# Kernel optimization log

Measured on AMD Instinct MI355X. Metric: run time of the kernel, lower is better.

## Reference

```python
import jax, jax.numpy as jnp
import numpy as np

N_NODES = 10000
N_EDGES = 640000
F_IN = 128
HID = 128
N_LAYERS = 3
N_ACT = 4096
NEG_SLOPE = 0.2


def setup_inputs() -> dict:
    key = jax.random.key(0)
    ks = jax.random.split(key, 16)
    s = 0.05
    return {
        "x": jax.random.normal(ks[0], (N_NODES, F_IN), jnp.float32),
        "edge_index": jax.random.randint(ks[1], (2, N_EDGES), 0, N_NODES, jnp.int64),
        "action_src": jax.random.randint(ks[2], (N_ACT,), 0, N_NODES, jnp.int64),
        "action_dst": jax.random.randint(ks[3], (N_ACT,), 0, N_NODES, jnp.int64),
        "action_type": jax.random.randint(ks[4], (N_ACT,), 0, 2, jnp.int32),
        "gat_W": jax.random.normal(ks[5], (N_LAYERS, HID, HID), jnp.float32) * s,
        "gat_asrc": jax.random.normal(ks[6], (N_LAYERS, HID), jnp.float32) * s,
        "gat_adst": jax.random.normal(ks[7], (N_LAYERS, HID), jnp.float32) * s,
        "gat_b": jax.random.normal(ks[8], (N_LAYERS, HID), jnp.float32) * s,
        "mlp_W1": jax.random.normal(ks[9], (2 * HID + 1, HID), jnp.float32) * s,
        "mlp_b1": jax.random.normal(ks[10], (HID,), jnp.float32) * s,
        "mlp_W2": jax.random.normal(ks[11], (HID, 1), jnp.float32) * s,
        "mlp_b2": jax.random.normal(ks[12], (1,), jnp.float32) * s,
    }


def _gat_layer(h, src, dst, W, a_src, a_dst, b, n_nodes):
    # PyG GATConv, heads=1: z = h W; e_ij = leaky_relu(a_src.z_j + a_dst.z_i)
    z = h @ W                                   # [N, HID]
    e = jax.nn.leaky_relu((z @ a_src)[src] + (z @ a_dst)[dst], NEG_SLOPE)  # [E+N]
    m = jax.ops.segment_max(e, dst, num_segments=n_nodes)
    m = jnp.where(jnp.isfinite(m), m, 0.0)
    ex = jnp.exp(e - m[dst])
    denom = jax.ops.segment_sum(ex, dst, num_segments=n_nodes)
    alpha = ex / denom[dst]                     # softmax over incoming edges
    out = jax.ops.segment_sum(alpha[:, None] * z[src], dst, num_segments=n_nodes)
    return out + b


def reference(x, edge_index, action_src, action_dst, action_type,
              gat_W, gat_asrc, gat_adst, gat_b,
              mlp_W1, mlp_b1, mlp_W2, mlp_b2):
    n = x.shape[0]
    loop = jnp.arange(n, dtype=edge_index.dtype)  # add_self_loops=True
    src = jnp.concatenate([edge_index[0], loop])
    dst = jnp.concatenate([edge_index[1], loop])
    h = x
    for l in range(N_LAYERS):
        h = jax.nn.relu(_gat_layer(h, src, dst, gat_W[l], gat_asrc[l], gat_adst[l], gat_b[l], n))
    # vectorized action scoring: [h[src], h[dst], type_flag] -> MLP -> scalar
    feat = jnp.concatenate(
        [h[action_src], h[action_dst], action_type.astype(h.dtype)[:, None]], axis=-1)
    hidden = jax.nn.relu(feat @ mlp_W1 + mlp_b1)
    scores = (hidden @ mlp_W2 + mlp_b2)[:, 0]   # [N_ACT]
    return scores
```

## Files before the change

kernel.cpp:

```cpp
#include <hip/hip_runtime.h>
#include <hip/hip_bf16.h>
#include <hip/hip_fp16.h>

#define N_NODES 10000
#define N_EDGES 640000
#define TOT_E   (N_EDGES + N_NODES)
#define HID     128
#define NEG_SLOPE 0.2f
#define N_ACT   4096

#define NBKT   250
#define NPB    40
#define P1_EPB 4096
#define P1_EPT 16
#define P1_BLOCKS 159
#define SLOTP  56
#define G_BLOCKS 313

__global__ __launch_bounds__(256) void part1_k(const int* __restrict__ ei,
                                               unsigned* __restrict__ bpart,
                                               int* __restrict__ bcnt) {
    __shared__ int hist[256];
    __shared__ int lofs[256];
    __shared__ int sc[256];
    __shared__ unsigned stage[P1_EPB];
    __shared__ unsigned char bkt_of[P1_EPB];
    int t = threadIdx.x;
    hist[t] = 0;
    __syncthreads();

    unsigned pk[P1_EPT];
    int bk[P1_EPT];
    int e0 = blockIdx.x * P1_EPB;
#pragma unroll
    for (int i = 0; i < P1_EPT; i++) {
        int e = e0 + i * 256 + t;
        if (e < TOT_E) {
            int src, dst;
            if (e < N_EDGES) { src = ei[e]; dst = ei[N_EDGES + e]; }
            else             { src = e - N_EDGES; dst = src; }
            pk[i] = ((unsigned)dst << 16) | (unsigned)src;
            bk[i] = dst / NPB;
            atomicAdd(&hist[bk[i]], 1);
        } else bk[i] = -1;
    }
    __syncthreads();
    int v = hist[t];
    sc[t] = v;
    __syncthreads();
    for (int o = 1; o < 256; o <<= 1) {
        int u = (t >= o) ? sc[t - o] : 0;
        __syncthreads();
        sc[t] += u;
        __syncthreads();
    }
    lofs[t] = sc[t] - v;
    bcnt[blockIdx.x * 256 + t] = v;
    hist[t] = 0;
    __syncthreads();
#pragma unroll
    for (int i = 0; i < P1_EPT; i++) {
        if (bk[i] >= 0) {
            int p = atomicAdd(&hist[bk[i]], 1);
            int slot = lofs[bk[i]] + p;
            stage[slot] = pk[i];
            bkt_of[slot] = (unsigned char)bk[i];
        }
    }
    __syncthreads();
    int nv = min(P1_EPB, TOT_E - e0);
    for (int s = t; s < nv; s += 256) {
        int b = bkt_of[s];
        bpart[b * (P1_BLOCKS * SLOTP) + blockIdx.x * SLOTP + (s - lofs[b])] = stage[s];
    }
}

__device__ __forceinline__ void agg_node(const __half2* __restrict__ z2,
                                         const float* __restrict__ zsi, float zdn,
                                         const int* __restrict__ csr, int o0, int deg,
                                         int lane, float& accx, float& accy, float& denom) {
    for (int base = 0; base < deg; base += 64) {
        int j = base + lane;
        int sreg = 0;
        float ex = 0.f;
        if (j < deg) {
            int s = csr[o0 + j];
            sreg = s;
            float e = zsi[s] + zdn;
            e = e > 0.f ? e : NEG_SLOPE * e;
            ex = __expf(e);
        }
        int cnt = min(64, deg - base);
        int nfull = cnt & ~7;
        int q = 0;
        if (nfull) {
            __half2 cur[8];
            float exc[8];
#pragma unroll
            for (int u = 0; u < 8; u++) {
                int sq = __builtin_amdgcn_readlane(sreg, u);
                exc[u] = __uint_as_float(
                    __builtin_amdgcn_readlane(__float_as_uint(ex), u));
                cur[u] = z2[sq * 64];
            }
            for (q = 8; q < nfull; q += 8) {
                __half2 nxt[8];
                float exn[8];
#pragma unroll
                for (int u = 0; u < 8; u++) {
                    int sq = __builtin_amdgcn_readlane(sreg, q + u);
                    exn[u] = __uint_as_float(
                        __builtin_amdgcn_readlane(__float_as_uint(ex), q + u));
                    nxt[u] = z2[sq * 64];
                }
#pragma unroll
                for (int u = 0; u < 8; u++) {
                    denom += exc[u];
                    float2 vf = __half22float2(cur[u]);
                    accx = fmaf(exc[u], vf.x, accx);
                    accy = fmaf(exc[u], vf.y, accy);
                    cur[u] = nxt[u];
                    exc[u] = exn[u];
                }
            }
#pragma unroll
            for (int u = 0; u < 8; u++) {
                denom += exc[u];
                float2 vf = __half22float2(cur[u]);
                accx = fmaf(exc[u], vf.x, accx);
                accy = fmaf(exc[u], vf.y, accy);
            }
            q = nfull;
        }
        for (; q < cnt; q++) {
            int sq = __builtin_amdgcn_readlane(sreg, q);
            float exq = __uint_as_float(
                __builtin_amdgcn_readlane(__float_as_uint(ex), q));
            denom += exq;
            float2 vf = __half22float2(z2[sq * 64]);
            accx = fmaf(exq, vf.x, accx);
            accy = fmaf(exq, vf.y, accy);
        }
    }
}

__device__ __forceinline__ void gload_lds16(const float* g, float* l) {
    __builtin_amdgcn_global_load_lds(
        (const __attribute__((address_space(1))) void*)g,
        (__attribute__((address_space(3))) void*)l, 16, 0, 0);
}

__global__ __launch_bounds__(256) void g2_k(const float* __restrict__ A,
                                            const float* __restrict__ W,
                                            const float* __restrict__ avs,
                                            const float* __restrict__ avd,
                                            __half* __restrict__ z16,
                                            float* __restrict__ zs,
                                            float* __restrict__ zd,
                                            const unsigned* __restrict__ bpart,
                                            const int* __restrict__ bcnt,
                                            int* __restrict__ csr,
                                            int* __restrict__ offs) {
    __shared__ float smem[20480];
    int t = threadIdx.x;

    if (blockIdx.x < G_BLOCKS) {
        float* As = smem;
        float* Ws = smem + 32 * HID;
        int w = t >> 6, lane = t & 63;
        int row0 = blockIdx.x * 32;
#pragma unroll
        for (int i = 0; i < 4; i++) {
            int chunk = w * 4 + i;
            long foff = (long)row0 * HID + chunk * 256;
            const float* g = ((foff + 256) <= (long)N_NODES * HID) ? (A + foff + lane * 4)
                                                                   : (A + lane * 4);
            gload_lds16(g, As + chunk * 256);
        }
#pragma unroll
        for (int i = 0; i < 16; i++) {
            int chunk = w * 16 + i;
            gload_lds16(W + chunk * 256 + lane * 4, Ws + chunk * 256);
        }
        __syncthreads();

        int tx = t & 31, ty = t >> 5;
        int r0 = ty * 4;
        float acc[4][4] = {{0.f}};
#pragma unroll 4
        for (int k4 = 0; k4 < 32; k4++) {
            float ak[4][4];
#pragma unroll
            for (int r = 0; r < 4; r++) {
                float4 a4 = *(const float4*)&As[(r0 + r) * HID + k4 * 4];
                ak[r][0] = a4.x; ak[r][1] = a4.y; ak[r][2] = a4.z; ak[r][3] = a4.w;
            }
            const float* Wb = &Ws[k4 * 4 * HID + tx * 4];
#pragma unroll
            for (int kk = 0; kk < 4; kk++) {
                float4 wv = *(const float4*)&Wb[kk * HID];
#pragma unroll
                for (int r = 0; r < 4; r++) {
                    acc[r][0] = fmaf(ak[r][kk], wv.x, acc[r][0]);
                    acc[r][1] = fmaf(ak[r][kk], wv.y, acc[r][1]);
                    acc[r][2] = fmaf(ak[r][kk], wv.z, acc[r][2]);
                    acc[r][3] = fmaf(ak[r][kk], wv.w, acc[r][3]);
                }
            }
        }
        float4 asv = *(const float4*)&avs[tx * 4];
        float4 adv = *(const float4*)&avd[tx * 4];
#pragma unroll
        for (int r = 0; r < 4; r++) {
            int row = row0 + r0 + r;
            if (row < N_NODES) {
                *(__half2*)&z16[row * HID + tx * 4]     = __floats2half2_rn(acc[r][0], acc[r][1]);
                *(__half2*)&z16[row * HID + tx * 4 + 2] = __floats2half2_rn(acc[r][2], acc[r][3]);
            }
            float ps = acc[r][0] * asv.x + acc[r][1] * asv.y + acc[r][2] * asv.z + acc[r][3] * asv.w;
            float pd = acc[r][0] * adv.x + acc[r][1] * adv.y + acc[r][2] * adv.z + acc[r][3] * adv.w;
#pragma unroll
            for (int o = 1; o < 32; o <<= 1) {
                ps += __shfl_xor(ps, o, 64);
                pd += __shfl_xor(pd, o, 64);
            }
            if (tx == 0 && row < N_NODES) { zs[row] = ps; zd[row] = pd; }
        }
    } else {
        int b = blockIdx.x - G_BLOCKS;
        unsigned* ebuf = (unsigned*)smem;
        int* sc    = (int*)(smem + 4096);
        int* Ls    = sc + 256;
        int* nhist = Ls + 256;
        __shared__ int bstart_s, cnt_s;

        int tot = 0;
        if (t < NBKT) {
            int t0 = 0, t1 = 0, t2 = 0, t3 = 0;
            int blk = 0;
            for (; blk + 4 <= P1_BLOCKS; blk += 4) {
                t0 += bcnt[(blk + 0) * 256 + t];
                t1 += bcnt[(blk + 1) * 256 + t];
                t2 += bcnt[(blk + 2) * 256 + t];
                t3 += bcnt[(blk + 3) * 256 + t];
            }
            for (; blk < P1_BLOCKS; blk++) t0 += bcnt[blk * 256 + t];
            tot = t0 + t1 + t2 + t3;
        }
        sc[t] = tot;
        __syncthreads();
        for (int o = 1; o < 256; o <<= 1) {
            int u = (t >= o) ? sc[t - o] : 0;
            __syncthreads();
            sc[t] += u;
            __syncthreads();
        }
        if (t == b) { bstart_s = sc[t] - tot; cnt_s = tot; }
        if (b == 0 && t == 255) offs[N_NODES] = sc[255];
        __syncthreads();

        int L = (t < P1_BLOCKS) ? bcnt[t * 256 + b] : 0;
        Ls[t] = L;
        sc[t] = L;
        __syncthreads();
        for (int o = 1; o < 256; o <<= 1) {
            int u = (t >= o) ? sc[t - o] : 0;
            __syncthreads();
            sc[t] += u;
            __syncthreads();
        }
        if (t < NPB) nhist[t] = 0;
        {
            int wv = t >> 6, lane = t & 63;
            const unsigned* bbase = bpart + b * (P1_BLOCKS * SLOTP);
            for (int r = wv; r < P1_BLOCKS; r += 4) {
                int Lr = Ls[r];
                if (lane < Lr) ebuf[(sc[r] - Lr) + lane] = bbase[r * SLOTP + lane];
            }
        }
        __syncthreads();

        int cnt = cnt_s;
        int n0 = b * NPB;
        for (int i = t; i < cnt; i += 256) atomicAdd(&nhist[(ebuf[i] >> 16) - n0], 1);
        __syncthreads();
        if (t < 64) {
            int v2 = (t < NPB) ? nhist[t] : 0;
            int s2 = v2;
            for (int o = 1; o < 64; o <<= 1) {
                int u = __shfl_up(s2, o, 64);
                if (t >= o) s2 += u;
            }
            if (t < NPB) {
                int ofs = bstart_s + s2 - v2;
                nhist[t] = ofs;
                offs[n0 + t] = ofs;
            }
        }
        __syncthreads();
        for (int i = t; i < cnt; i += 256) {
            unsigned pk = ebuf[i];
            int p = atomicAdd(&nhist[(pk >> 16) - n0], 1);
            csr[p] = pk & 0xFFFF;
        }
    }
}


__global__ __launch_bounds__(256) void fuse_k(const __half* __restrict__ z16i,
                                              const float* __restrict__ zsi,
                                              const float* __restrict__ zdi,
                                              const int* __restrict__ offs,
                                              const int* __restrict__ csr,
                                              const float* __restrict__ bprev,
                                              const float* __restrict__ W,
                                              const float* __restrict__ avs,
                                              const float* __restrict__ avd,
                                              __half* __restrict__ z16o,
                                              float* __restrict__ zso,
                                              float* __restrict__ zdo) {
    __shared__ float hT[8][HID];
    __shared__ float Wc[2][32 * HID];
    int t = threadIdx.x;
    int w = t >> 6, lane = t & 63;
    int n0 = blockIdx.x * 8;
    float4 wreg[4];
    {
        const float4* Wg = (const float4*)W;
#pragma unroll
        for (int i = 0; i < 4; i++) wreg[i] = Wg[t + 256 * i];
    }
    const __half2* z2 = (const __half2*)z16i + lane;

    float2 bv = *(const float2*)&bprev[2 * lane];
#pragma unroll
    for (int i = 0; i < 2; i++) {
        int ln = w * 2 + i;
        int n = n0 + ln;
        int o0 = offs[n];
        int deg = offs[n + 1] - o0;
        float zdn = zdi[n];
        float accx = 0.f, accy = 0.f, denom = 0.f;
        agg_node(z2, zsi, zdn, csr, o0, deg, lane, accx, accy, denom);
        float inv = 1.0f / denom;
        float vx = accx * inv + bv.x;
        float vy = accy * inv + bv.y;
        float2 hv;
        hv.x = vx > 0.f ? vx : 0.f;
        hv.y = vy > 0.f ? vy : 0.f;
        *(float2*)&hT[ln][2 * lane] = hv;
    }

    int tx = t & 31, ty = t >> 5;
    float acc[4] = {0.f, 0.f, 0.f, 0.f};
    for (int c = 0; c < 4; c++) {
        float4* dstb = (float4*)Wc[c & 1];
#pragma unroll
        for (int i = 0; i < 4; i++) dstb[t + 256 * i] = wreg[i];
        __syncthreads();
        if (c + 1 < 4) {
            const float4* Wg = (const float4*)(W + (c + 1) * 32 * HID);
#pragma unroll
            for (int i = 0; i < 4; i++) wreg[i] = Wg[t + 256 * i];
        }
        const float* Wb = Wc[c & 1];
        const float* h0 = &hT[ty][c * 32];
#pragma unroll 8
        for (int kk = 0; kk < 32; kk++) {
            float f0 = h0[kk];
            float4 wv = *(const float4*)&Wb[kk * HID + tx * 4];
            acc[0] = fmaf(f0, wv.x, acc[0]);
            acc[1] = fmaf(f0, wv.y, acc[1]);
            acc[2] = fmaf(f0, wv.z, acc[2]);
            acc[3] = fmaf(f0, wv.w, acc[3]);
        }
    }
    float4 asv = *(const float4*)&avs[tx * 4];
    float4 adv = *(const float4*)&avd[tx * 4];
    int row = n0 + ty;
    *(__half2*)&z16o[row * HID + tx * 4]     = __floats2half2_rn(acc[0], acc[1]);
    *(__half2*)&z16o[row * HID + tx * 4 + 2] = __floats2half2_rn(acc[2], acc[3]);
    float ps = acc[0] * asv.x + acc[1] * asv.y + acc[2] * asv.z + acc[3] * asv.w;
    float pd = acc[0] * adv.x + acc[1] * adv.y + acc[2] * adv.z + acc[3] * adv.w;
#pragma unroll
    for (int o = 1; o < 32; o <<= 1) {
        ps += __shfl_xor(ps, o, 64);
        pd += __shfl_xor(pd, o, 64);
    }
    if (tx == 0) { zso[row] = ps; zdo[row] = pd; }
}


__global__ __launch_bounds__(256) void agg_k(const __half* __restrict__ z16,
                                             const float* __restrict__ zs,
                                             const float* __restrict__ zd,
                                             const int* __restrict__ offs,
                                             const int* __restrict__ csr,
                                             const float* __restrict__ b,
                                             float* __restrict__ hout) {
    int t = threadIdx.x;
    int w = t >> 6, lane = t & 63;
    int n = blockIdx.x * 4 + w;
    if (n >= N_NODES) return;
    int o0 = offs[n];
    int deg = offs[n + 1] - o0;
    float zdn = zd[n];
    const __half2* z2 = (const __half2*)z16 + lane;
    float accx = 0.f, accy = 0.f, denom = 0.f;
    agg_node(z2, zs, zdn, csr, o0, deg, lane, accx, accy, denom);
    float inv = 1.0f / denom;
    float2 bv = *(const float2*)&b[2 * lane];
    float vx = accx * inv + bv.x;
    float vy = accy * inv + bv.y;
    float2 o;
    o.x = vx > 0.f ? vx : 0.f;
    o.y = vy > 0.f ? vy : 0.f;
    *(float2*)&hout[n * HID + 2 * lane] = o;
}


#define SC_APB 16

__global__ __launch_bounds__(256) void score_k(const float* __restrict__ h,
                                               const int* __restrict__ asrc,
                                               const int* __restrict__ adst,
                                               const int* __restrict__ atype,
                                               const float* __restrict__ W1,
                                               const float* __restrict__ b1,
                                               const float* __restrict__ W2,
                                               const float* __restrict__ b2,
                                               float* __restrict__ out) {
    __shared__ float featT[257][SC_APB + 1];
    __shared__ float Wc[2][32 * HID];
    int t = threadIdx.x;
    int a0 = blockIdx.x * SC_APB;

    float4 wreg[4];
    {
        const float4* Wg = (const float4*)W1;
#pragma unroll
        for (int i = 0; i < 4; i++) wreg[i] = Wg[t + 256 * i];
    }
    for (int idx = t; idx < SC_APB * 128; idx += 256) {
        int a = idx >> 7, c = idx & 127;
        featT[c][a]       = h[asrc[a0 + a] * HID + c];
        featT[128 + c][a] = h[adst[a0 + a] * HID + c];
    }
    if (t < SC_APB) featT[256][t] = (float)atype[a0 + t];

    int cg = t & 31, ap = t >> 5;
    float4 bv = *(const float4*)&b1[cg * 4];
    float acc0[4] = {bv.x, bv.y, bv.z, bv.w};
    float acc1[4] = {bv.x, bv.y, bv.z, bv.w};

    for (int c = 0; c < 8; c++) {
        float4* dstb = (float4*)Wc[c & 1];
#pragma unroll
        for (int i = 0; i < 4; i++) dstb[t + 256 * i] = wreg[i];
        __syncthreads();
        if (c + 1 < 8) {
            const float4* Wg = (const float4*)(W1 + (c + 1) * 32 * HID);
#pragma unroll
            for (int i = 0; i < 4; i++) wreg[i] = Wg[t + 256 * i];
        }
        const float* Wb = Wc[c & 1];
        const float* fT = &featT[c * 32][0];
#pragma unroll 8
        for (int kk = 0; kk < 32; kk++) {
            float4 wv = *(const float4*)&Wb[kk * HID + cg * 4];
            float f0 = fT[kk * (SC_APB + 1) + ap * 2];
            float f1 = fT[kk * (SC_APB + 1) + ap * 2 + 1];
            acc0[0] = fmaf(f0, wv.x, acc0[0]);
            acc0[1] = fmaf(f0, wv.y, acc0[1]);
            acc0[2] = fmaf(f0, wv.z, acc0[2]);
            acc0[3] = fmaf(f0, wv.w, acc0[3]);
            acc1[0] = fmaf(f1, wv.x, acc1[0]);
            acc1[1] = fmaf(f1, wv.y, acc1[1]);
            acc1[2] = fmaf(f1, wv.z, acc1[2]);
            acc1[3] = fmaf(f1, wv.w, acc1[3]);
        }
    }
    {
        float4 wv = *(const float4*)&W1[256 * HID + cg * 4];
        float f0 = featT[256][ap * 2];
        float f1 = featT[256][ap * 2 + 1];
        acc0[0] = fmaf(f0, wv.x, acc0[0]); acc0[1] = fmaf(f0, wv.y, acc0[1]);
        acc0[2] = fmaf(f0, wv.z, acc0[2]); acc0[3] = fmaf(f0, wv.w, acc0[3]);
        acc1[0] = fmaf(f1, wv.x, acc1[0]); acc1[1] = fmaf(f1, wv.y, acc1[1]);
        acc1[2] = fmaf(f1, wv.z, acc1[2]); acc1[3] = fmaf(f1, wv.w, acc1[3]);
    }
    float4 w2v = *(const float4*)&W2[cg * 4];
    float v0 = 0.f, v1 = 0.f;
    v0 += (acc0[0] > 0.f ? acc0[0] : 0.f) * w2v.x;
    v0 += (acc0[1] > 0.f ? acc0[1] : 0.f) * w2v.y;
    v0 += (acc0[2] > 0.f ? acc0[2] : 0.f) * w2v.z;
    v0 += (acc0[3] > 0.f ? acc0[3] : 0.f) * w2v.w;
    v1 += (acc1[0] > 0.f ? acc1[0] : 0.f) * w2v.x;
    v1 += (acc1[1] > 0.f ? acc1[1] : 0.f) * w2v.y;
    v1 += (acc1[2] > 0.f ? acc1[2] : 0.f) * w2v.z;
    v1 += (acc1[3] > 0.f ? acc1[3] : 0.f) * w2v.w;
#pragma unroll
    for (int o = 1; o < 32; o <<= 1) {
        v0 += __shfl_xor(v0, o, 64);
        v1 += __shfl_xor(v1, o, 64);
    }
    if (cg == 0) {
        out[a0 + ap * 2]     = v0 + b2[0];
        out[a0 + ap * 2 + 1] = v1 + b2[0];
    }
}


extern "C" void kernel_launch(void* const* d_in, const int* in_sizes, int n_in,
                              void* d_out, int out_size, void* d_ws, size_t ws_size,
                              hipStream_t stream) {
    const float* x   = (const float*)d_in[0];
    const int* ei    = (const int*)d_in[1];
    const int* asrc  = (const int*)d_in[2];
    const int* adst  = (const int*)d_in[3];
    const int* atype = (const int*)d_in[4];
    const float* gW  = (const float*)d_in[5];
    const float* gas = (const float*)d_in[6];
    const float* gad = (const float*)d_in[7];
    const float* gb  = (const float*)d_in[8];
    const float* W1  = (const float*)d_in[9];
    const float* b1  = (const float*)d_in[10];
    const float* W2  = (const float*)d_in[11];
    const float* b2  = (const float*)d_in[12];
    float* out = (float*)d_out;

    __half* z16A = (__half*)d_ws;
    __half* z16B = z16A + N_NODES * HID;
    float* h3   = (float*)(z16B + N_NODES * HID);
    float* zsA  = h3 + N_NODES * HID;
    float* zdA  = zsA + N_NODES;
    float* zsB  = zdA + N_NODES;
    float* zdB  = zsB + N_NODES;
    int* offs   = (int*)(zdB + N_NODES);
    int* csr    = offs + (N_NODES + 1);
    int* bcnt   = csr + TOT_E;
    unsigned* bpart = (unsigned*)(bcnt + P1_BLOCKS * 256);

    part1_k<<<P1_BLOCKS, 256, 0, stream>>>(ei, bpart, bcnt);
    g2_k<<<G_BLOCKS + NBKT, 256, 0, stream>>>(x, gW, gas, gad, z16A, zsA, zdA,
                                              bpart, bcnt, csr, offs);

    fuse_k<<<N_NODES / 8, 256, 0, stream>>>(z16A, zsA, zdA, offs, csr, gb,
                                            gW + 1 * HID * HID, gas + 1 * HID, gad + 1 * HID,
                                            z16B, zsB, zdB);
    fuse_k<<<N_NODES / 8, 256, 0, stream>>>(z16B, zsB, zdB, offs, csr, gb + 1 * HID,
                                            gW + 2 * HID * HID, gas + 2 * HID, gad + 2 * HID,
                                            z16A, zsA, zdA);
    agg_k<<<(N_NODES + 3) / 4, 256, 0, stream>>>(z16A, zsA, zdA, offs, csr,
                                                 gb + 2 * HID, h3);
    score_k<<<N_ACT / SC_APB, 256, 0, stream>>>(h3, asrc, adst, atype,
                                                W1, b1, W2, b2, out);
}
```

Measured before the change: 217.6 us.

## Enlarge fused GAT node tile and stream full W into LDS asynchronously

Each fused aggregate+transform block now handles 24 nodes instead of 8. It loads the entire 128x128 weight matrix into shared memory with asynchronous global-to-LDS loads issued before the aggregation, so the copy overlaps the gather. The matmul is register-tiled to 3 rows per thread to amortise weight reads. This cuts redundant per-block weight traffic but raises LDS use per block and reduces block count, which may lower occupancy for the latency-bound gather phase.

After: 231.2 us. +6.3%, slower.

```diff
diff --git a/kernel.cpp b/kernel.cpp
--- a/kernel.cpp
+++ b/kernel.cpp
@@ -16,6 +16,8 @@
 #define P1_BLOCKS 159
 #define SLOTP  56
 #define G_BLOCKS 313
+#define FUSE_NPT 24
+#define FUSE_B  417
 
 __global__ __launch_bounds__(256) void part1_k(const int* __restrict__ ei,
                                                unsigned* __restrict__ bpart,
@@ -99,8 +101,7 @@
 #pragma unroll
             for (int u = 0; u < 8; u++) {
                 int sq = __builtin_amdgcn_readlane(sreg, u);
-                exc[u] = __uint_as_float(
-                    __builtin_amdgcn_readlane(__float_as_uint(ex), u));
+                exc[u] = __uint_as_float(__builtin_amdgcn_readlane(__float_as_uint(ex), u));
                 cur[u] = z2[sq * 64];
             }
             for (q = 8; q < nfull; q += 8) {
@@ -109,8 +110,7 @@
 #pragma unroll
                 for (int u = 0; u < 8; u++) {
                     int sq = __builtin_amdgcn_readlane(sreg, q + u);
-                    exn[u] = __uint_as_float(
-                        __builtin_amdgcn_readlane(__float_as_uint(ex), q + u));
+                    exn[u] = __uint_as_float(__builtin_amdgcn_readlane(__float_as_uint(ex), q + u));
                     nxt[u] = z2[sq * 64];
                 }
 #pragma unroll
@@ -134,8 +134,7 @@
         }
         for (; q < cnt; q++) {
             int sq = __builtin_amdgcn_readlane(sreg, q);
-            float exq = __uint_as_float(
-                __builtin_amdgcn_readlane(__float_as_uint(ex), q));
+            float exq = __uint_as_float(__builtin_amdgcn_readlane(__float_as_uint(ex), q));
             denom += exq;
             float2 vf = __half22float2(z2[sq * 64]);
             accx = fmaf(exq, vf.x, accx);
@@ -306,7 +305,6 @@
     }
 }
 
-
 __global__ __launch_bounds__(256) void fuse_k(const __half* __restrict__ z16i,
                                               const float* __restrict__ zsi,
                                               const float* __restrict__ zdi,
@@ -319,75 +317,82 @@
                                               __half* __restrict__ z16o,
                                               float* __restrict__ zso,
                                               float* __restrict__ zdo) {
-    __shared__ float hT[8][HID];
-    __shared__ float Wc[2][32 * HID];
+    __shared__ float hT[FUSE_NPT][HID];
+    __shared__ float Ws[HID * HID];
     int t = threadIdx.x;
     int w = t >> 6, lane = t & 63;
-    int n0 = blockIdx.x * 8;
-    float4 wreg[4];
-    {
-        const float4* Wg = (const float4*)W;
-#pragma unroll
-        for (int i = 0; i < 4; i++) wreg[i] = Wg[t + 256 * i];
-    }
+    int n0 = blockIdx.x * FUSE_NPT;
+
+#pragma unroll
+    for (int i = 0; i < 16; i++) {
+        int chunk = w * 16 + i;
+        gload_lds16(W + chunk * 256 + lane * 4, Ws + chunk * 256);
+    }
+
     const __half2* z2 = (const __half2*)z16i + lane;
-
     float2 bv = *(const float2*)&bprev[2 * lane];
 #pragma unroll
-    for (int i = 0; i < 2; i++) {
-        int ln = w * 2 + i;
+    for (int i = 0; i < 6; i++) {
+        int ln = w * 6 + i;
         int n = n0 + ln;
-        int o0 = offs[n];
-        int deg = offs[n + 1] - o0;
-        float zdn = zdi[n];
-        float accx = 0.f, accy = 0.f, denom = 0.f;
-        agg_node(z2, zsi, zdn, csr, o0, deg, lane, accx, accy, denom);
-        float inv = 1.0f / denom;
-        float vx = accx * inv + bv.x;
-        float vy = accy * inv + bv.y;
-        float2 hv;
-        hv.x = vx > 0.f ? vx : 0.f;
-        hv.y = vy > 0.f ? vy : 0.f;
-        *(float2*)&hT[ln][2 * lane] = hv;
-    }
+        if (n < N_NODES) {
+            int o0 = offs[n];
+            int deg = offs[n + 1] - o0;
+            float zdn = zdi[n];
+            float accx = 0.f, accy = 0.f, denom = 0.f;
+            agg_node(z2, zsi, zdn, csr, o0, deg, lane, accx, accy, denom);
+            float inv = 1.0f / denom;
+            float vx = accx * inv + bv.x;
+            float vy = accy * inv + bv.y;
+            float2 hv;
+            hv.x = vx > 0.f ? vx : 0.f;
+            hv.y = vy > 0.f ? vy : 0.f;
+            *(float2*)&hT[ln][2 * lane] = hv;
+        }
+    }
+    __syncthreads();
 
     int tx = t & 31, ty = t >> 5;
-    float acc[4] = {0.f, 0.f, 0.f, 0.f};
-    for (int c = 0; c < 4; c++) {
-        float4* dstb = (float4*)Wc[c & 1];
-#pragma unroll
-        for (int i = 0; i < 4; i++) dstb[t + 256 * i] = wreg[i];
-        __syncthreads();
-        if (c + 1 < 4) {
-            const float4* Wg = (const float4*)(W + (c + 1) * 32 * HID);
-#pragma unroll
-            for (int i = 0; i < 4; i++) wreg[i] = Wg[t + 256 * i];
-        }
-        const float* Wb = Wc[c & 1];
-        const float* h0 = &hT[ty][c * 32];
-#pragma unroll 8
-        for (int kk = 0; kk < 32; kk++) {
-            float f0 = h0[kk];
-            float4 wv = *(const float4*)&Wb[kk * HID + tx * 4];
-            acc[0] = fmaf(f0, wv.x, acc[0]);
-            acc[1] = fmaf(f0, wv.y, acc[1]);
-            acc[2] = fmaf(f0, wv.z, acc[2]);
-            acc[3] = fmaf(f0, wv.w, acc[3]);
+    float acc[3][4] = {{0.f}};
+#pragma unroll 4
+    for (int k4 = 0; k4 < 32; k4++) {
+        float4 av[3];
+#pragma unroll
+        for (int u = 0; u < 3; u++)
+            av[u] = *(const float4*)&hT[ty * 3 + u][k4 * 4];
+        const float* Wb = &Ws[k4 * 4 * HID + tx * 4];
+#pragma unroll
+        for (int kk = 0; kk < 4; kk++) {
+            float4 wv = *(const float4*)&Wb[kk * HID];
+#pragma unroll
+            for (int u = 0; u < 3; u++) {
+                float f = (kk == 0) ? av[u].x : (kk == 1) ? av[u].y
+                         : (kk == 2) ? av[u].z : av[u].w;
+                acc[u][0] = fmaf(f, wv.x, acc[u][0]);
+                acc[u][1] = fmaf(f, wv.y, acc[u][1]);
+                acc[u][2] = fmaf(f, wv.z, acc[u][2]);
+                acc[u][3] = fmaf(f, wv.w, acc[u][3]);
+            }
         }
     }
     float4 asv = *(const float4*)&avs[tx * 4];
     float4 adv = *(const float4*)&avd[tx * 4];
-    int row = n0 + ty;
-    *(__half2*)&z16o[row * HID + tx * 4]     = __floats2half2_rn(acc[0], acc[1]);
-    *(__half2*)&z16o[row * HID + tx * 4 + 2] = __floats2half2_rn(acc[2], acc[3]);
-    float ps = acc[0] * asv.x + acc[1] * asv.y + acc[2] * asv.z + acc[3] * asv.w;
-    float pd = acc[0] * adv.x + acc[1] * adv.y + acc[2] * adv.z + acc[3] * adv.w;
-#pragma unroll
-    for (int o = 1; o < 32; o <<= 1) {
-        ps += __shfl_xor(ps, o, 64);
-        pd += __shfl_xor(pd, o, 64);
-    }
-    if (tx == 0) { zso[row] = ps; zdo[row] = pd; }
+#pragma unroll
+    for (int u = 0; u < 3; u++) {
+        int row = n0 + ty * 3 + u;
+        float ps = acc[u][0] * asv.x + acc[u][1] * asv.y + acc[u][2] * asv.z + acc[u][3] * asv.w;
+        float pd = acc[u][0] * adv.x + acc[u][1] * adv.y + acc[u][2] * adv.z + acc[u][3] * adv.w;
+#pragma unroll
+        for (int o = 1; o < 32; o <<= 1) {
+            ps += __shfl_xor(ps, o, 64);
+            pd += __shfl_xor(pd, o, 64);
+        }
+        if (row < N_NODES) {
+            *(__half2*)&z16o[row * HID + tx * 4]     = __floats2half2_rn(acc[u][0], acc[u][1]);
+            *(__half2*)&z16o[row * HID + tx * 4 + 2] = __floats2half2_rn(acc[u][2], acc[u][3]);
+            if (tx == 0) { zso[row] = ps; zdo[row] = pd; }
+        }
+    }
 }
 
 
@@ -545,12 +550,12 @@
     g2_k<<<G_BLOCKS + NBKT, 256, 0, stream>>>(x, gW, gas, gad, z16A, zsA, zdA,
                                               bpart, bcnt, csr, offs);
 
-    fuse_k<<<N_NODES / 8, 256, 0, stream>>>(z16A, zsA, zdA, offs, csr, gb,
-                                            gW + 1 * HID * HID, gas + 1 * HID, gad + 1 * HID,
-                                            z16B, zsB, zdB);
-    fuse_k<<<N_NODES / 8, 256, 0, stream>>>(z16B, zsB, zdB, offs, csr, gb + 1 * HID,
-                                            gW + 2 * HID * HID, gas + 2 * HID, gad + 2 * HID,
-                                            z16A, zsA, zdA);
+    fuse_k<<<FUSE_B, 256, 0, stream>>>(z16A, zsA, zdA, offs, csr, gb,
+                                       gW + 1 * HID * HID, gas + 1 * HID, gad + 1 * HID,
+                                       z16B, zsB, zdB);
+    fuse_k<<<FUSE_B, 256, 0, stream>>>(z16B, zsB, zdB, offs, csr, gb + 1 * HID,
+                                       gW + 2 * HID * HID, gas + 2 * HID, gad + 2 * HID,
+                                       z16A, zsA, zdA);
     agg_k<<<(N_NODES + 3) / 4, 256, 0, stream>>>(z16A, zsA, zdA, offs, csr,
                                                  gb + 2 * HID, h3);
     score_k<<<N_ACT / SC_APB, 256, 0, stream>>>(h3, asrc, adst, atype,
```

## Split fused aggregate+GEMM into separate grid-stride agg and LDS-tiled GEMM kernels

Applied to the files above, without the earlier changes.

Replaces the per-layer fused aggregation+projection kernel with two kernels: a grid-stride aggregation kernel with launch bounds for higher occupancy, and the LDS-tiled GEMM body reused from the first layer. The software-pipelined gather loop in agg_node is simplified to a plain unrolled loop. This aims to remove the poor GEMM efficiency of 8-row tiles and the per-block W reloads, at the cost of extra launches and an fp32 H round trip through memory.

After: 212.4 us. 2.4% less time.

```diff
diff --git a/kernel.cpp b/kernel.cpp
--- a/kernel.cpp
+++ b/kernel.cpp
@@ -16,6 +16,7 @@
 #define P1_BLOCKS 159
 #define SLOTP  56
 #define G_BLOCKS 313
+#define AGG_B  2048
 
 __global__ __launch_bounds__(256) void part1_k(const int* __restrict__ ei,
                                                unsigned* __restrict__ bpart,
@@ -91,46 +92,18 @@
             ex = __expf(e);
         }
         int cnt = min(64, deg - base);
-        int nfull = cnt & ~7;
         int q = 0;
-        if (nfull) {
-            __half2 cur[8];
-            float exc[8];
+        for (; q + 8 <= cnt; q += 8) {
 #pragma unroll
             for (int u = 0; u < 8; u++) {
-                int sq = __builtin_amdgcn_readlane(sreg, u);
-                exc[u] = __uint_as_float(
-                    __builtin_amdgcn_readlane(__float_as_uint(ex), u));
-                cur[u] = z2[sq * 64];
-            }
-            for (q = 8; q < nfull; q += 8) {
-                __half2 nxt[8];
-                float exn[8];
-#pragma unroll
-                for (int u = 0; u < 8; u++) {
-                    int sq = __builtin_amdgcn_readlane(sreg, q + u);
-                    exn[u] = __uint_as_float(
-                        __builtin_amdgcn_readlane(__float_as_uint(ex), q + u));
-                    nxt[u] = z2[sq * 64];
-                }
-#pragma unroll
-                for (int u = 0; u < 8; u++) {
-                    denom += exc[u];
-                    float2 vf = __half22float2(cur[u]);
-                    accx = fmaf(exc[u], vf.x, accx);
-                    accy = fmaf(exc[u], vf.y, accy);
-                    cur[u] = nxt[u];
-                    exc[u] = exn[u];
-                }
-            }
-#pragma unroll
-            for (int u = 0; u < 8; u++) {
-                denom += exc[u];
-                float2 vf = __half22float2(cur[u]);
-                accx = fmaf(exc[u], vf.x, accx);
-                accy = fmaf(exc[u], vf.y, accy);
-            }
-            q = nfull;
+                int sq = __builtin_amdgcn_readlane(sreg, q + u);
+                float exq = __uint_as_float(
+                    __builtin_amdgcn_readlane(__float_as_uint(ex), q + u));
+                denom += exq;
+                float2 vf = __half22float2(z2[sq * 64]);
+                accx = fmaf(exq, vf.x, accx);
+                accy = fmaf(exq, vf.y, accy);
+            }
         }
         for (; q < cnt; q++) {
             int sq = __builtin_amdgcn_readlane(sreg, q);
@@ -148,6 +121,77 @@
     __builtin_amdgcn_global_load_lds(
         (const __attribute__((address_space(1))) void*)g,
         (__attribute__((address_space(3))) void*)l, 16, 0, 0);
+}
+
+__device__ __forceinline__ void gemm_body(const float* __restrict__ A,
+                                          const float* __restrict__ W,
+                                          const float* __restrict__ avs,
+                                          const float* __restrict__ avd,
+                                          __half* __restrict__ z16,
+                                          float* __restrict__ zs,
+                                          float* __restrict__ zd,
+                                          float* smem, int blk, int t) {
+    float* As = smem;
+    float* Ws = smem + 32 * HID;
+    int w = t >> 6, lane = t & 63;
+    int row0 = blk * 32;
+#pragma unroll
+    for (int i = 0; i < 4; i++) {
+        int chunk = w * 4 + i;
+        long foff = (long)row0 * HID + chunk * 256;
+        const float* g = ((foff + 256) <= (long)N_NODES * HID) ? (A + foff + lane * 4)
+                                                               : (A + lane * 4);
+        gload_lds16(g, As + chunk * 256);
+    }
+#pragma unroll
+    for (int i = 0; i < 16; i++) {
+        int chunk = w * 16 + i;
+        gload_lds16(W + chunk * 256 + lane * 4, Ws + chunk * 256);
+    }
+    __syncthreads();
+
+    int tx = t & 31, ty = t >> 5;
+    int r0 = ty * 4;
+    float acc[4][4] = {{0.f}};
+#pragma unroll 4
+    for (int k4 = 0; k4 < 32; k4++) {
+        float ak[4][4];
+#pragma unroll
+        for (int r = 0; r < 4; r++) {
+            float4 a4 = *(const float4*)&As[(r0 + r) * HID + k4 * 4];
+            ak[r][0] = a4.x; ak[r][1] = a4.y; ak[r][2] = a4.z; ak[r][3] = a4.w;
+        }
+        const float* Wb = &Ws[k4 * 4 * HID + tx * 4];
+#pragma unroll
+        for (int kk = 0; kk < 4; kk++) {
+            float4 wv = *(const float4*)&Wb[kk * HID];
+#pragma unroll
+            for (int r = 0; r < 4; r++) {
+                acc[r][0] = fmaf(ak[r][kk], wv.x, acc[r][0]);
+                acc[r][1] = fmaf(ak[r][kk], wv.y, acc[r][1]);
+                acc[r][2] = fmaf(ak[r][kk], wv.z, acc[r][2]);
+                acc[r][3] = fmaf(ak[r][kk], wv.w, acc[r][3]);
+            }
+        }
+    }
+    float4 asv = *(const float4*)&avs[tx * 4];
+    float4 adv = *(const float4*)&avd[tx * 4];
+#pragma unroll
+    for (int r = 0; r < 4; r++) {
+        int row = row0 + r0 + r;
+        if (row < N_NODES) {
+            *(__half2*)&z16[row * HID + tx * 4]     = __floats2half2_rn(acc[r][0], acc[r][1]);
+            *(__half2*)&z16[row * HID + tx * 4 + 2] = __floats2half2_rn(acc[r][2], acc[r][3]);
+        }
+        float ps = acc[r][0] * asv.x + acc[r][1] * asv.y + acc[r][2] * asv.z + acc[r][3] * asv.w;
+        float pd = acc[r][0] * adv.x + acc[r][1] * adv.y + acc[r][2] * adv.z + acc[r][3] * adv.w;
+#pragma unroll
+        for (int o = 1; o < 32; o <<= 1) {
+            ps += __shfl_xor(ps, o, 64);
+            pd += __shfl_xor(pd, o, 64);
+        }
+        if (tx == 0 && row < N_NODES) { zs[row] = ps; zd[row] = pd; }
+    }
 }
 
 __global__ __launch_bounds__(256) void g2_k(const float* __restrict__ A,
@@ -165,67 +209,7 @@
     int t = threadIdx.x;
 
     if (blockIdx.x < G_BLOCKS) {
-        float* As = smem;
-        float* Ws = smem + 32 * HID;
-        int w = t >> 6, lane = t & 63;
-        int row0 = blockIdx.x * 32;
-#pragma unroll
-        for (int i = 0; i < 4; i++) {
-            int chunk = w * 4 + i;
-            long foff = (long)row0 * HID + chunk * 256;
-            const float* g = ((foff + 256) <= (long)N_NODES * HID) ? (A + foff + lane * 4)
-                                                                   : (A + lane * 4);
-            gload_lds16(g, As + chunk * 256);
-        }
-#pragma unroll
-        for (int i = 0; i < 16; i++) {
-            int chunk = w * 16 + i;
-            gload_lds16(W + chunk * 256 + lane * 4, Ws + chunk * 256);
-        }
-        __syncthreads();
-
-        int tx = t & 31, ty = t >> 5;
-        int r0 = ty * 4;
-        float acc[4][4] = {{0.f}};
-#pragma unroll 4
-        for (int k4 = 0; k4 < 32; k4++) {
-            float ak[4][4];
-#pragma unroll
-            for (int r = 0; r < 4; r++) {
-                float4 a4 = *(const float4*)&As[(r0 + r) * HID + k4 * 4];
-                ak[r][0] = a4.x; ak[r][1] = a4.y; ak[r][2] = a4.z; ak[r][3] = a4.w;
-            }
-            const float* Wb = &Ws[k4 * 4 * HID + tx * 4];
-#pragma unroll
-            for (int kk = 0; kk < 4; kk++) {
-                float4 wv = *(const float4*)&Wb[kk * HID];
-#pragma unroll
-                for (int r = 0; r < 4; r++) {
-                    acc[r][0] = fmaf(ak[r][kk], wv.x, acc[r][0]);
-                    acc[r][1] = fmaf(ak[r][kk], wv.y, acc[r][1]);
-                    acc[r][2] = fmaf(ak[r][kk], wv.z, acc[r][2]);
-                    acc[r][3] = fmaf(ak[r][kk], wv.w, acc[r][3]);
-                }
-            }
-        }
-        float4 asv = *(const float4*)&avs[tx * 4];
-        float4 adv = *(const float4*)&avd[tx * 4];
-#pragma unroll
-        for (int r = 0; r < 4; r++) {
-            int row = row0 + r0 + r;
-            if (row < N_NODES) {
-                *(__half2*)&z16[row * HID + tx * 4]     = __floats2half2_rn(acc[r][0], acc[r][1]);
-                *(__half2*)&z16[row * HID + tx * 4 + 2] = __floats2half2_rn(acc[r][2], acc[r][3]);
-            }
-            float ps = acc[r][0] * asv.x + acc[r][1] * asv.y + acc[r][2] * asv.z + acc[r][3] * asv.w;
-            float pd = acc[r][0] * adv.x + acc[r][1] * adv.y + acc[r][2] * adv.z + acc[r][3] * adv.w;
-#pragma unroll
-            for (int o = 1; o < 32; o <<= 1) {
-                ps += __shfl_xor(ps, o, 64);
-                pd += __shfl_xor(pd, o, 64);
-            }
-            if (tx == 0 && row < N_NODES) { zs[row] = ps; zd[row] = pd; }
-        }
+        gemm_body(A, W, avs, avd, z16, zs, zd, smem, blockIdx.x, t);
     } else {
         int b = blockIdx.x - G_BLOCKS;
         unsigned* ebuf = (unsigned*)smem;
@@ -306,116 +290,42 @@
     }
 }
 
-
-__global__ __launch_bounds__(256) void fuse_k(const __half* __restrict__ z16i,
-                                              const float* __restrict__ zsi,
-                                              const float* __restrict__ zdi,
-                                              const int* __restrict__ offs,
-                                              const int* __restrict__ csr,
-                                              const float* __restrict__ bprev,
-                                              const float* __restrict__ W,
-                                              const float* __restrict__ avs,
-                                              const float* __restrict__ avd,
-                                              __half* __restrict__ z16o,
-                                              float* __restrict__ zso,
-                                              float* __restrict__ zdo) {
-    __shared__ float hT[8][HID];
-    __shared__ float Wc[2][32 * HID];
+__global__ __launch_bounds__(256) void gemmh_k(const float* __restrict__ A,
+                                               const float* __restrict__ W,
+                                               const float* __restrict__ avs,
+                                               const float* __restrict__ avd,
+                                               __half* __restrict__ z16,
+                                               float* __restrict__ zs,
+                                               float* __restrict__ zd) {
+    __shared__ float smem[20480];
+    gemm_body(A, W, avs, avd, z16, zs, zd, smem, blockIdx.x, threadIdx.x);
+}
+
+__global__ __launch_bounds__(256, 8) void agg_k(const __half* __restrict__ z16,
+                                                const float* __restrict__ zs,
+                                                const float* __restrict__ zd,
+                                                const int* __restrict__ offs,
+                                                const int* __restrict__ csr,
+                                                const float* __restrict__ b,
+                                                float* __restrict__ hout) {
     int t = threadIdx.x;
     int w = t >> 6, lane = t & 63;
-    int n0 = blockIdx.x * 8;
-    float4 wreg[4];
-    {
-        const float4* Wg = (const float4*)W;
-#pragma unroll
-        for (int i = 0; i < 4; i++) wreg[i] = Wg[t + 256 * i];
-    }
-    const __half2* z2 = (const __half2*)z16i + lane;
-
-    float2 bv = *(const float2*)&bprev[2 * lane];
-#pragma unroll
-    for (int i = 0; i < 2; i++) {
-        int ln = w * 2 + i;
-        int n = n0 + ln;
+    const __half2* z2 = (const __half2*)z16 + lane;
+    float2 bv = *(const float2*)&b[2 * lane];
+    for (int n = blockIdx.x * 4 + w; n < N_NODES; n += AGG_B * 4) {
         int o0 = offs[n];
         int deg = offs[n + 1] - o0;
-        float zdn = zdi[n];
+        float zdn = zd[n];
         float accx = 0.f, accy = 0.f, denom = 0.f;
-        agg_node(z2, zsi, zdn, csr, o0, deg, lane, accx, accy, denom);
+        agg_node(z2, zs, zdn, csr, o0, deg, lane, accx, accy, denom);
         float inv = 1.0f / denom;
         float vx = accx * inv + bv.x;
         float vy = accy * inv + bv.y;
-        float2 hv;
-        hv.x = vx > 0.f ? vx : 0.f;
-        hv.y = vy > 0.f ? vy : 0.f;
-        *(float2*)&hT[ln][2 * lane] = hv;
-    }
-
-    int tx = t & 31, ty = t >> 5;
-    float acc[4] = {0.f, 0.f, 0.f, 0.f};
-    for (int c = 0; c < 4; c++) {
-        float4* dstb = (float4*)Wc[c & 1];
-#pragma unroll
-        for (int i = 0; i < 4; i++) dstb[t + 256 * i] = wreg[i];
-        __syncthreads();
-        if (c + 1 < 4) {
-            const float4* Wg = (const float4*)(W + (c + 1) * 32 * HID);
-#pragma unroll
-            for (int i = 0; i < 4; i++) wreg[i] = Wg[t + 256 * i];
-        }
-        const float* Wb = Wc[c & 1];
-        const float* h0 = &hT[ty][c * 32];
-#pragma unroll 8
-        for (int kk = 0; kk < 32; kk++) {
-            float f0 = h0[kk];
-            float4 wv = *(const float4*)&Wb[kk * HID + tx * 4];
-            acc[0] = fmaf(f0, wv.x, acc[0]);
-            acc[1] = fmaf(f0, wv.y, acc[1]);
-            acc[2] = fmaf(f0, wv.z, acc[2]);
-            acc[3] = fmaf(f0, wv.w, acc[3]);
-        }
-    }
-    float4 asv = *(const float4*)&avs[tx * 4];
-    float4 adv = *(const float4*)&avd[tx * 4];
-    int row = n0 + ty;
-    *(__half2*)&z16o[row * HID + tx * 4]     = __floats2half2_rn(acc[0], acc[1]);
-    *(__half2*)&z16o[row * HID + tx * 4 + 2] = __floats2half2_rn(acc[2], acc[3]);
-    float ps = acc[0] * asv.x + acc[1] * asv.y + acc[2] * asv.z + acc[3] * asv.w;
-    float pd = acc[0] * adv.x + acc[1] * adv.y + acc[2] * adv.z + acc[3] * adv.w;
-#pragma unroll
-    for (int o = 1; o < 32; o <<= 1) {
-        ps += __shfl_xor(ps, o, 64);
-        pd += __shfl_xor(pd, o, 64);
-    }
-    if (tx == 0) { zso[row] = ps; zdo[row] = pd; }
-}
-
-
-__global__ __launch_bounds__(256) void agg_k(const __half* __restrict__ z16,
-                                             const float* __restrict__ zs,
-                                             const float* __restrict__ zd,
-                                             const int* __restrict__ offs,
-                                             const int* __restrict__ csr,
-                                             const float* __restrict__ b,
-                                             float* __restrict__ hout) {
-    int t = threadIdx.x;
-    int w = t >> 6, lane = t & 63;
-    int n = blockIdx.x * 4 + w;
-    if (n >= N_NODES) return;
-    int o0 = offs[n];
-    int deg = offs[n + 1] - o0;
-    float zdn = zd[n];
-    const __half2* z2 = (const __half2*)z16 + lane;
-    float accx = 0.f, accy = 0.f, denom = 0.f;
-    agg_node(z2, zs, zdn, csr, o0, deg, lane, accx, accy, denom);
-    float inv = 1.0f / denom;
-    float2 bv = *(const float2*)&b[2 * lane];
-    float vx = accx * inv + bv.x;
-    float vy = accy * inv + bv.y;
-    float2 o;
-    o.x = vx > 0.f ? vx : 0.f;
-    o.y = vy > 0.f ? vy : 0.f;
-    *(float2*)&hout[n * HID + 2 * lane] = o;
+        float2 o;
+        o.x = vx > 0.f ? vx : 0.f;
+        o.y = vy > 0.f ? vy : 0.f;
+        *(float2*)&hout[n * HID + 2 * lane] = o;
+    }
 }
 
 
@@ -531,8 +441,8 @@
 
     __half* z16A = (__half*)d_ws;
     __half* z16B = z16A + N_NODES * HID;
-    float* h3   = (float*)(z16B + N_NODES * HID);
-    float* zsA  = h3 + N_NODES * HID;
+    float* H    = (float*)(z16B + N_NODES * HID);
+    float* zsA  = H + N_NODES * HID;
     float* zdA  = zsA + N_NODES;
     float* zsB  = zdA + N_NODES;
     float* zdB  = zsB + N_NODES;
@@ -545,14 +455,14 @@
     g2_k<<<G_BLOCKS + NBKT, 256, 0, stream>>>(x, gW, gas, gad, z16A, zsA, zdA,
                                               bpart, bcnt, csr, offs);
 
-    fuse_k<<<N_NODES / 8, 256, 0, stream>>>(z16A, zsA, zdA, offs, csr, gb,
-                                            gW + 1 * HID * HID, gas + 1 * HID, gad + 1 * HID,
-                                            z16B, zsB, zdB);
-    fuse_k<<<N_NODES / 8, 256, 0, stream>>>(z16B, zsB, zdB, offs, csr, gb + 1 * HID,
-                                            gW + 2 * HID * HID, gas + 2 * HID, gad + 2 * HID,
-                                            z16A, zsA, zdA);
-    agg_k<<<(N_NODES + 3) / 4, 256, 0, stream>>>(z16A, zsA, zdA, offs, csr,
-                                                 gb + 2 * HID, h3);
-    score_k<<<N_ACT / SC_APB, 256, 0, stream>>>(h3, asrc, adst, atype,
+    agg_k<<<AGG_B, 256, 0, stream>>>(z16A, zsA, zdA, offs, csr, gb, H);
+    gemmh_k<<<G_BLOCKS, 256, 0, stream>>>(H, gW + 1 * HID * HID, gas + 1 * HID,
+                                          gad + 1 * HID, z16B, zsB, zdB);
+    agg_k<<<AGG_B, 256, 0, stream>>>(z16B, zsB, zdB, offs, csr, gb + 1 * HID, H);
+    gemmh_k<<<G_BLOCKS, 256, 0, stream>>>(H, gW + 2 * HID * HID, gas + 2 * HID,
+                                          gad + 2 * HID, z16A, zsA, zdA);
+    agg_k<<<AGG_B, 256, 0, stream>>>(z16A, zsA, zdA, offs, csr, gb + 2 * HID, H);
+
+    score_k<<<N_ACT / SC_APB, 256, 0, stream>>>(H, asrc, adst, atype,
                                                 W1, b1, W2, b2, out);
 }
```
